# Kernel optimization log

Hardware: AMD Instinct MI355X
Metric: run time of the kernel (lower is better)

Reference implementation:

```python
import jax, jax.numpy as jnp
import numpy as np

L, B, E, H = 1024, 8, 1024, 16


def setup_inputs() -> dict:
    key = jax.random.key(0)
    k1, k2, k3, k4, k5 = jax.random.split(key, 5)
    scale = 1.0 / np.sqrt(E)
    return {
        "x": jax.random.normal(k1, (L, B, E), dtype=jnp.float32),
        "in_proj_weight": jax.random.normal(k2, (3 * E, E), dtype=jnp.float32) * scale,
        "in_proj_bias": jax.random.normal(k3, (3 * E,), dtype=jnp.float32) * 0.01,
        "out_proj_weight": jax.random.normal(k4, (E, E), dtype=jnp.float32) * scale,
        "out_proj_bias": jax.random.normal(k5, (E,), dtype=jnp.float32) * 0.01,
        "num_heads": H,
    }


def reference(x, in_proj_weight, in_proj_bias, out_proj_weight, out_proj_bias, num_heads):
    # x: [L, B, E] (tgt_len, batch, embed_dim), self-attention path of
    # multi_head_attention_func (no masks, no bias_k/v, no add_zero_attn,
    # dropout_p=0 / eval mode).
    Lq, Bq, Eq = x.shape
    hd = Eq // num_heads
    scaling = float(hd) ** -0.5
    # fused qkv projection: linear(x, in_proj_weight, in_proj_bias).chunk(3)
    qkv = x @ in_proj_weight.T + in_proj_bias  # [L, B, 3E]
    q, k, v = jnp.split(qkv, 3, axis=-1)
    q = q * scaling
    def to_heads(t):  # [L, B, E] -> [B*H, L, hd]
        return t.reshape(Lq, Bq * num_heads, hd).transpose(1, 0, 2)
    q, k, v = to_heads(q), to_heads(k), to_heads(v)
    # explicit QK^T -> softmax -> PV (naive attention, as in the source)
    scores = jnp.einsum('bqd,bkd->bqk', q, k)      # [B*H, L, L]
    attn = jax.nn.softmax(scores, axis=-1)
    out = jnp.einsum('bqk,bkd->bqd', attn, v)      # [B*H, L, hd]
    out = out.transpose(1, 0, 2).reshape(Lq, Bq, Eq)
    out = out @ out_proj_weight.T + out_proj_bias  # [L, B, E]
    return out
```

## Files before the change

### kernel.cpp

```cpp
#include <hip/hip_runtime.h>

#define L_DIM 1024
#define B_DIM 8
#define E_DIM 1024
#define H_DIM 16
#define HD 64
#define BH_DIM (B_DIM * H_DIM)

typedef float f32x4 __attribute__((ext_vector_type(4)));
typedef _Float16 f16_t;
typedef f16_t f16x4 __attribute__((ext_vector_type(4)));
typedef f16_t f16x8 __attribute__((ext_vector_type(8)));

static __device__ __forceinline__ void gld16(const void* g, void* l) {
  __builtin_amdgcn_global_load_lds(
      (const __attribute__((address_space(1))) unsigned int*)g,
      (__attribute__((address_space(3))) unsigned int*)l, 16, 0, 0);
}

__global__ __launch_bounds__(256) void convert_f16(
    const float* __restrict__ x, const float* __restrict__ wi,
    const float* __restrict__ wo, f16_t* __restrict__ x16,
    f16_t* __restrict__ wi16, f16_t* __restrict__ wo16) {
  const int NX = (L_DIM * B_DIM * E_DIM) / 4;
  const int NWI = (3 * E_DIM * E_DIM) / 4;
  const int NWO = (E_DIM * E_DIM) / 4;
  const int total = NX + NWI + NWO;
  for (int i = blockIdx.x * blockDim.x + threadIdx.x; i < total;
       i += gridDim.x * blockDim.x) {
    const float4* src; f16_t* dst; int j;
    if (i < NX)            { src = (const float4*)x;  dst = x16;  j = i; }
    else if (i < NX + NWI) { src = (const float4*)wi; dst = wi16; j = i - NX; }
    else                   { src = (const float4*)wo; dst = wo16; j = i - NX - NWI; }
    const float4 v = src[j];
    f16x4 h = {(f16_t)v.x, (f16_t)v.y, (f16_t)v.z, (f16_t)v.w};
    *(f16x4*)(dst + (size_t)j * 4) = h;
  }
}

template <int MODE>
__global__ __launch_bounds__(256, 2) void gemm_f16(
    const f16_t* __restrict__ A, const f16_t* __restrict__ B,
    const float* __restrict__ bias, void* __restrict__ O0v,
    void* __restrict__ O1v, void* __restrict__ O2v) {
  constexpr int K = 1024;
  __shared__ __align__(16) f16_t As[128 * 32];
  __shared__ __align__(16) f16_t Bs[128 * 32];

  const int tid = threadIdx.x;
  const int lane = tid & 63;
  const int wave = tid >> 6;
  const int wm = (wave & 1) * 64;
  const int wn = (wave >> 1) * 64;
  const int quad = lane >> 4;
  const int l16 = lane & 15;
  const int m0 = blockIdx.y * 128;
  const int n0 = blockIdx.x * 128;

  const int cr = tid >> 2;
  const int cc = (tid & 3) * 8;

  f32x4 acc[4][4] = {};

  for (int k0 = 0; k0 < K; k0 += 32) {
    __syncthreads();
    gld16(A + (size_t)(m0 + cr) * K + k0 + cc,      As + tid * 8);
    gld16(A + (size_t)(m0 + 64 + cr) * K + k0 + cc, As + 2048 + tid * 8);
    gld16(B + (size_t)(n0 + cr) * K + k0 + cc,      Bs + tid * 8);
    gld16(B + (size_t)(n0 + 64 + cr) * K + k0 + cc, Bs + 2048 + tid * 8);
    __syncthreads();

    f16x8 af[4], bf[4];
#pragma unroll
    for (int t = 0; t < 4; ++t) {
      af[t] = *(const f16x8*)&As[(wm + t * 16 + l16) * 32 + quad * 8];
      bf[t] = *(const f16x8*)&Bs[(wn + t * 16 + l16) * 32 + quad * 8];
    }
#pragma unroll
    for (int i = 0; i < 4; ++i)
#pragma unroll
      for (int j = 0; j < 4; ++j)
        acc[i][j] = __builtin_amdgcn_mfma_f32_16x16x32_f16(af[i], bf[j], acc[i][j], 0, 0, 0);
  }

#pragma unroll
  for (int i = 0; i < 4; ++i) {
    const int mbase = m0 + wm + i * 16 + quad * 4;
#pragma unroll
    for (int j = 0; j < 4; ++j) {
      const int n = n0 + wn + j * 16 + l16;
      const float bv = bias[n];
      if (MODE == 0) {
        f16_t* O0 = (f16_t*)O0v; f16_t* O1 = (f16_t*)O1v; f16_t* O2 = (f16_t*)O2v;
        const int chunk = n >> 10;
        const int e = n & 1023;
        const int h = e >> 6;
        const int d = e & 63;
#pragma unroll
        for (int r = 0; r < 4; ++r) {
          const int m = mbase + r;
          const int l = m >> 3, b = m & 7;
          const size_t idx = ((size_t)(b * H_DIM + h) * L_DIM + l) * HD + d;
          const float val = acc[i][j][r] + bv;
          if (chunk == 0)      O0[idx] = (f16_t)(val * 0.125f);
          else if (chunk == 1) O1[idx] = (f16_t)val;
          else                 O2[idx] = (f16_t)val;
        }
      } else {
        float* O0 = (float*)O0v;
#pragma unroll
        for (int r = 0; r < 4; ++r) {
          const int m = mbase + r;
          O0[(size_t)m * E_DIM + n] = acc[i][j][r] + bv;
        }
      }
    }
  }
}

__global__ __launch_bounds__(256, 2) void attn_f16(
    const f16_t* __restrict__ Q, const f16_t* __restrict__ K,
    const f16_t* __restrict__ V, f16_t* __restrict__ O) {
  constexpr int KSTR = 70;
  __shared__ __align__(16) f16_t Ks[64 * KSTR];
  __shared__ __align__(16) f16_t Vs[64 * KSTR];
  __shared__ float Ls[4][64];

  const int tid = threadIdx.x;
  const int lane = tid & 63;
  const int w = tid >> 6;
  const int quad = lane >> 4;
  const int l16 = lane & 15;
  const int bh = blockIdx.y;
  const int q0 = blockIdx.x * 256 + w * 64;

  const f16_t* Qb = Q + (size_t)bh * L_DIM * HD;
  const f16_t* Kb = K + (size_t)bh * L_DIM * HD;
  const f16_t* Vb = V + (size_t)bh * L_DIM * HD;

  f16x8 qf[4][2];
#pragma unroll
  for (int nt = 0; nt < 4; ++nt)
#pragma unroll
    for (int kc = 0; kc < 2; ++kc)
      qf[nt][kc] = *(const f16x8*)(Qb + (size_t)(q0 + nt * 16 + l16) * HD + kc * 32 + quad * 8);

  f32x4 oacc[4][4] = {};
  float rsum[4] = {0.0f, 0.0f, 0.0f, 0.0f};

  const int sr = tid >> 3;
  const int sc8 = (tid & 7) * 8;
  const int va = tid & 31;
  const int vg = tid >> 5;
  const int rA = (l16 >> 2) * 8 + (l16 & 3);

  for (int kt = 0; kt < 16; ++kt) {
    __syncthreads();
    {
      const f16_t* kp = Kb + (size_t)(kt * 64) * HD;
#pragma unroll
      for (int rr = 0; rr < 2; ++rr) {
        const int row = sr + rr * 32;
        *(f16x8*)&Ks[row * KSTR + sc8] = *(const f16x8*)(kp + (size_t)row * HD + sc8);
      }
      const f16_t* vp = Vb + (size_t)(kt * 64 + vg * 8) * HD + 2 * va;
      unsigned int vd[8];
#pragma unroll
      for (int i = 0; i < 8; ++i) vd[i] = *(const unsigned int*)(vp + (size_t)i * HD);
      union { unsigned int u[4]; f16x8 v; } lo, hi;
#pragma unroll
      for (int i = 0; i < 4; ++i) {
        lo.u[i] = (vd[2 * i] & 0xffffu) | (vd[2 * i + 1] << 16);
        hi.u[i] = (vd[2 * i] >> 16) | (vd[2 * i + 1] & 0xffff0000u);
      }
      *(f16x8*)&Vs[(2 * va) * KSTR + vg * 8] = lo.v;
      *(f16x8*)&Vs[(2 * va + 1) * KSTR + vg * 8] = hi.v;
    }
    __syncthreads();

#pragma unroll
    for (int c = 0; c < 2; ++c) {
      f32x4 sc[2][4] = {};
#pragma unroll
      for (int h = 0; h < 2; ++h) {
        const int row = c * 32 + h * 4 + rA;
#pragma unroll
        for (int kc = 0; kc < 2; ++kc) {
          const f16x8 ka = *(const f16x8*)&Ks[row * KSTR + kc * 32 + quad * 8];
#pragma unroll
          for (int nt = 0; nt < 4; ++nt)
            sc[h][nt] = __builtin_amdgcn_mfma_f32_16x16x32_f16(ka, qf[nt][kc], sc[h][nt], 0, 0, 0);
        }
      }

      f16x8 pa[4];
#pragma unroll
      for (int nt = 0; nt < 4; ++nt)
#pragma unroll
        for (int h = 0; h < 2; ++h)
#pragma unroll
          for (int r = 0; r < 4; ++r) {
            const float e = __expf(sc[h][nt][r]);
            rsum[nt] += e;
            pa[nt][h * 4 + r] = (f16_t)e;
          }

#pragma unroll
      for (int nd = 0; nd < 4; ++nd) {
        const f16x8 vb = *(const f16x8*)&Vs[(nd * 16 + l16) * KSTR + c * 32 + quad * 8];
#pragma unroll
        for (int nt = 0; nt < 4; ++nt)
          oacc[nt][nd] = __builtin_amdgcn_mfma_f32_16x16x32_f16(pa[nt], vb, oacc[nt][nd], 0, 0, 0);
      }
    }
  }

#pragma unroll
  for (int nt = 0; nt < 4; ++nt) {
    float rs = rsum[nt];
    rs += __shfl_xor(rs, 16); rs += __shfl_xor(rs, 32);
    if (quad == 0) Ls[w][nt * 16 + l16] = rs;
  }
  asm volatile("s_waitcnt lgkmcnt(0)" ::: "memory");

  const int b = bh >> 4;
  const int h = bh & 15;
#pragma unroll
  for (int nt = 0; nt < 4; ++nt)
#pragma unroll
    for (int r = 0; r < 4; ++r) {
      const int ql = nt * 16 + quad * 4 + r;
      const float inv = 1.0f / Ls[w][ql];
      const int qrow = q0 + ql;
#pragma unroll
      for (int nd = 0; nd < 4; ++nd) {
        const int d = nd * 16 + l16;
        O[((size_t)qrow * B_DIM + b) * E_DIM + h * HD + d] = (f16_t)(oacc[nt][nd][r] * inv);
      }
    }
}

extern "C" void kernel_launch(void* const* d_in, const int* in_sizes, int n_in,
                              void* d_out, int out_size, void* d_ws, size_t ws_size,
                              hipStream_t stream) {
  const float* x     = (const float*)d_in[0];
  const float* w_in  = (const float*)d_in[1];
  const float* b_in  = (const float*)d_in[2];
  const float* w_out = (const float*)d_in[3];
  const float* b_out = (const float*)d_in[4];

  const size_t TS = (size_t)BH_DIM * L_DIM * HD;
  f16_t* q16  = (f16_t*)d_ws;
  f16_t* k16  = q16 + TS;
  f16_t* v16  = k16 + TS;
  f16_t* x16  = v16 + TS;
  f16_t* wi16 = x16 + TS;
  f16_t* wo16 = wi16 + (size_t)3 * E_DIM * E_DIM;
  f16_t* ao16 = x16;

  convert_f16<<<4096, 256, 0, stream>>>(x, w_in, w_out, x16, wi16, wo16);
  gemm_f16<0><<<dim3(24, 64), 256, 0, stream>>>(x16, wi16, b_in, q16, k16, v16);
  attn_f16<<<dim3(4, 128), 256, 0, stream>>>(q16, k16, v16, ao16);
  gemm_f16<1><<<dim3(8, 64), 256, 0, stream>>>(ao16, wo16, b_out, d_out, nullptr, nullptr);
}
```

Measured before the change: 239.7 us.

## Add a pipelined 256x256-tile QKV GEMM with swizzled double-buffered LDS

Replaces the 128x128 QKV projection GEMM with a new 512-thread kernel. Each block computes a 256x256 tile with a K step of 64, using double-buffered LDS filled by asynchronous global_load_lds. Loads for the next tile are interleaved with MFMA phases, gated by vmcnt waits and barriers, with s_setprio raised around the MFMA bursts. It also XOR-swizzles LDS to avoid bank conflicts and remaps block ids for better L2 locality. The aim is more operand reuse per tile and overlap of memory with compute. The cost is about 128KB of LDS per block, which limits occupancy to one block per CU, plus a more fragile hand-written barrier schedule.

```diff
diff --git a/kernel.cpp b/kernel.cpp
--- a/kernel.cpp
+++ b/kernel.cpp
@@ -38,6 +38,135 @@
   }
 }
 
+
+#define GQ_FENCE asm volatile("" ::: "memory")
+#define GQ_BARRIER do { GQ_FENCE; __builtin_amdgcn_s_barrier(); GQ_FENCE; } while (0)
+#define GQ_LGKM0 do { asm volatile("s_waitcnt lgkmcnt(0)" ::: "memory"); \
+                      __builtin_amdgcn_sched_barrier(0); } while (0)
+#define GQ_VMCNT4 asm volatile("s_waitcnt vmcnt(4)" ::: "memory")
+
+#define STAGE_A(d, ht, kt) do {                                              \
+    gld16(Asrc + (size_t)(ht) * (128 * 1024) + (kt) * 64,                    \
+          &As[(d) * 16384 + (ht) * 8192 + tid * 8]);                         \
+    gld16(Asrc + (size_t)(ht) * (128 * 1024) + 64 * 1024 + (kt) * 64,        \
+          &As[(d) * 16384 + (ht) * 8192 + 4096 + tid * 8]);                  \
+  } while (0)
+#define STAGE_B(d, ht, kt) do {                                              \
+    gld16(Bsrc + (size_t)(ht) * (128 * 1024) + (kt) * 64,                    \
+          &Bs[(d) * 16384 + (ht) * 8192 + tid * 8]);                         \
+    gld16(Bsrc + (size_t)(ht) * (128 * 1024) + 64 * 1024 + (kt) * 64,        \
+          &Bs[(d) * 16384 + (ht) * 8192 + 4096 + tid * 8]);                  \
+  } while (0)
+
+static __device__ __forceinline__ const f16x8* fp16frag(
+    const f16_t* tile, int r, int ks, int quad, int l16) {
+  const int bo = (r * 128 + ks * 64 + quad * 16) ^ ((l16 & 7) << 4);
+  return (const f16x8*)((const char*)tile + bo);
+}
+
+#define GQ_PHASE(d, g, STAGE_STMT, ENDWAIT) do {                             \
+    f16x8 af_[2][2];                                                         \
+    _Pragma("unroll") for (int f_ = 0; f_ < 2; ++f_)                         \
+      _Pragma("unroll") for (int ks_ = 0; ks_ < 2; ++ks_)                    \
+        af_[f_][ks_] = *fp16frag(&As[(d) * 16384],                           \
+            wr * 128 + ((g) * 2 + f_) * 16 + l16, ks_, quad, l16);           \
+    if ((g) == 0) {                                                          \
+      _Pragma("unroll") for (int c_ = 0; c_ < 4; ++c_)                       \
+        _Pragma("unroll") for (int ks_ = 0; ks_ < 2; ++ks_)                  \
+          bf[c_][ks_] = *fp16frag(&Bs[(d) * 16384],                          \
+              wc * 64 + c_ * 16 + l16, ks_, quad, l16);                      \
+    }                                                                        \
+    STAGE_STMT;                                                              \
+    GQ_BARRIER;                                                              \
+    GQ_LGKM0;                                                                \
+    __builtin_amdgcn_s_setprio(1);                                           \
+    _Pragma("unroll") for (int f_ = 0; f_ < 2; ++f_)                         \
+      _Pragma("unroll") for (int c_ = 0; c_ < 4; ++c_)                       \
+        _Pragma("unroll") for (int ks_ = 0; ks_ < 2; ++ks_)                  \
+          acc[(g) * 2 + f_][c_] = __builtin_amdgcn_mfma_f32_16x16x32_f16(    \
+              af_[f_][ks_], bf[c_][ks_], acc[(g) * 2 + f_][c_], 0, 0, 0);    \
+    __builtin_amdgcn_s_setprio(0);                                           \
+    ENDWAIT;                                                                 \
+    GQ_BARRIER;                                                              \
+  } while (0)
+
+__global__ __launch_bounds__(512, 2) void gemm_qkv(
+    const f16_t* __restrict__ A, const f16_t* __restrict__ B,
+    const float* __restrict__ bias, f16_t* __restrict__ Oq,
+    f16_t* __restrict__ Ok, f16_t* __restrict__ Ov) {
+  constexpr int K = 1024;
+  constexpr int NT = K / 64;
+  __shared__ __align__(16) f16_t As[2 * 16384];
+  __shared__ __align__(16) f16_t Bs[2 * 16384];
+
+  const int tid = threadIdx.x;
+  const int lane = tid & 63;
+  const int w = tid >> 6;
+  const int wr = w >> 2;
+  const int wc = w & 3;
+  const int quad = lane >> 4;
+  const int l16 = lane & 15;
+
+  const int bid = blockIdx.x;
+  const int wg = (bid & 7) * 48 + (bid >> 3);
+  const int tn = wg >> 5;
+  const int tm = wg & 31;
+  const int m0 = tm * 256;
+  const int n0 = tn * 256;
+
+  const int srow = tid >> 3;
+  const int scol = ((tid & 7) ^ (srow & 7)) * 8;
+  const f16_t* Asrc = A + (size_t)(m0 + srow) * K + scol;
+  const f16_t* Bsrc = B + (size_t)(n0 + srow) * K + scol;
+
+  f32x4 acc[8][4] = {};
+  f16x8 bf[4][2];
+
+  STAGE_A(0, 0, 0); STAGE_A(0, 1, 0);
+  STAGE_B(0, 0, 0); STAGE_B(0, 1, 0);
+  STAGE_B(1, 0, 1); STAGE_B(1, 1, 1);
+  GQ_VMCNT4;
+  GQ_BARRIER;
+
+  for (int it = 0; it < 8; ++it) {
+    const int t1 = 2 * it + 1;
+    const int ta = (2 * it + 2 < NT) ? 2 * it + 2 : NT - 1;
+    const int tb = (2 * it + 3 < NT) ? 2 * it + 3 : NT - 1;
+    GQ_PHASE(0, 0, STAGE_A(1, 0, t1), );
+    GQ_PHASE(0, 1, STAGE_A(1, 1, t1), );
+    GQ_PHASE(0, 2, STAGE_B(0, 0, ta), );
+    GQ_PHASE(0, 3, STAGE_B(0, 1, ta), GQ_VMCNT4);
+    GQ_PHASE(1, 0, STAGE_A(0, 0, ta), );
+    GQ_PHASE(1, 1, STAGE_A(0, 1, ta), );
+    GQ_PHASE(1, 2, STAGE_B(1, 0, tb), );
+    GQ_PHASE(1, 3, STAGE_B(1, 1, tb), GQ_VMCNT4);
+  }
+
+#pragma unroll
+  for (int i = 0; i < 8; ++i) {
+    const int mbase = m0 + wr * 128 + i * 16 + quad * 4;
+#pragma unroll
+    for (int c = 0; c < 4; ++c) {
+      const int n = n0 + wc * 64 + c * 16 + l16;
+      const float bv = bias[n];
+      const int chunk = n >> 10;
+      const int e = n & 1023;
+      const int h = e >> 6;
+      const int d = e & 63;
+#pragma unroll
+      for (int r = 0; r < 4; ++r) {
+        const int m = mbase + r;
+        const int l = m >> 3, b = m & 7;
+        const size_t idx = ((size_t)(b * H_DIM + h) * L_DIM + l) * HD + d;
+        const float val = acc[i][c][r] + bv;
+        if (chunk == 0)      Oq[idx] = (f16_t)(val * 0.125f);
+        else if (chunk == 1) Ok[idx] = (f16_t)val;
+        else                 Ov[idx] = (f16_t)val;
+      }
+    }
+  }
+}
+
 template <int MODE>
 __global__ __launch_bounds__(256, 2) void gemm_f16(
     const f16_t* __restrict__ A, const f16_t* __restrict__ B,
@@ -70,17 +199,17 @@
     gld16(B + (size_t)(n0 + 64 + cr) * K + k0 + cc, Bs + 2048 + tid * 8);
     __syncthreads();
 
-    f16x8 af[4], bf[4];
+    f16x8 af[4], bfr[4];
 #pragma unroll
     for (int t = 0; t < 4; ++t) {
-      af[t] = *(const f16x8*)&As[(wm + t * 16 + l16) * 32 + quad * 8];
-      bf[t] = *(const f16x8*)&Bs[(wn + t * 16 + l16) * 32 + quad * 8];
+      af[t]  = *(const f16x8*)&As[(wm + t * 16 + l16) * 32 + quad * 8];
+      bfr[t] = *(const f16x8*)&Bs[(wn + t * 16 + l16) * 32 + quad * 8];
     }
 #pragma unroll
     for (int i = 0; i < 4; ++i)
 #pragma unroll
       for (int j = 0; j < 4; ++j)
-        acc[i][j] = __builtin_amdgcn_mfma_f32_16x16x32_f16(af[i], bf[j], acc[i][j], 0, 0, 0);
+        acc[i][j] = __builtin_amdgcn_mfma_f32_16x16x32_f16(af[i], bfr[j], acc[i][j], 0, 0, 0);
   }
 
 #pragma unroll
@@ -259,7 +388,7 @@
   f16_t* ao16 = x16;
 
   convert_f16<<<4096, 256, 0, stream>>>(x, w_in, w_out, x16, wi16, wo16);
-  gemm_f16<0><<<dim3(24, 64), 256, 0, stream>>>(x16, wi16, b_in, q16, k16, v16);
+  gemm_qkv<<<384, 512, 0, stream>>>(x16, wi16, b_in, q16, k16, v16);
   attn_f16<<<dim3(4, 128), 256, 0, stream>>>(q16, k16, v16, ao16);
   gemm_f16<1><<<dim3(8, 64), 256, 0, stream>>>(ao16, wo16, b_out, d_out, nullptr, nullptr);
 }
```

After: 240.7 us. No clear change (+0.4%).

## Add double-buffered swizzled QKV GEMM with XCD-aware tile mapping

Applied to the files above, without the earlier changes.

Replaces the QKV projection GEMM with a new kernel that uses BK=64 tiles, two LDS buffers with async global-to-LDS prefetch two stages ahead, XOR-swizzled LDS layout to avoid bank conflicts, MFMA priority raising, and a block-id remap that groups M tiles per XCD for L2 reuse. The aim is to hide global load latency behind MFMA work and improve cache locality in the largest GEMM. It doubles LDS use per block (64KB), which may limit occupancy to the two blocks the launch bounds request.

```diff
diff --git a/kernel.cpp b/kernel.cpp
--- a/kernel.cpp
+++ b/kernel.cpp
@@ -38,6 +38,117 @@
   }
 }
 
+
+#define GQ_FENCE asm volatile("" ::: "memory")
+#define GQ_BARRIER do { GQ_FENCE; __builtin_amdgcn_s_barrier(); GQ_FENCE; } while (0)
+#define VMW(n) asm volatile("s_waitcnt vmcnt(" #n ")" ::: "memory")
+
+static __device__ __forceinline__ const f16x8* fp16frag(
+    const f16_t* tile, int r, int ks, int quad, int l16) {
+  const int bo = (r * 128 + ks * 64 + quad * 16) ^ ((l16 & 7) << 4);
+  return (const f16x8*)((const char*)tile + bo);
+}
+
+__global__ __launch_bounds__(256, 2) void gemm_qkv(
+    const f16_t* __restrict__ A, const f16_t* __restrict__ B,
+    const float* __restrict__ bias, f16_t* __restrict__ Oq,
+    f16_t* __restrict__ Ok, f16_t* __restrict__ Ov) {
+  constexpr int K = 1024;
+  __shared__ __align__(16) f16_t As[2 * 8192];
+  __shared__ __align__(16) f16_t Bs[2 * 8192];
+
+  const int tid = threadIdx.x;
+  const int lane = tid & 63;
+  const int w = tid >> 6;
+  const int wm = (w & 1) * 64;
+  const int wn = (w >> 1) * 64;
+  const int quad = lane >> 4;
+  const int l16 = lane & 15;
+
+  const int bid = blockIdx.x;
+  const int xcd = bid & 7;
+  const int idx = bid >> 3;
+  const int tm = xcd * 8 + (idx & 7);
+  const int tn = idx >> 3;
+  const int m0 = tm * 128;
+  const int n0 = tn * 128;
+
+  const int r8 = tid >> 3;
+  const int gsw = (tid & 7) ^ (r8 & 7);
+  const f16_t* Abase = A + (size_t)(m0 + r8) * K + gsw * 8;
+  const f16_t* Bbase = B + (size_t)(n0 + r8) * K + gsw * 8;
+
+#define STAGE(kt, d) do {                                                    \
+    _Pragma("unroll") for (int s_ = 0; s_ < 4; ++s_)                         \
+      gld16(Abase + (size_t)s_ * 32 * K + (kt) * 64,                         \
+            &As[(d) * 8192 + s_ * 2048 + tid * 8]);                          \
+    _Pragma("unroll") for (int s_ = 0; s_ < 4; ++s_)                         \
+      gld16(Bbase + (size_t)s_ * 32 * K + (kt) * 64,                         \
+            &Bs[(d) * 8192 + s_ * 2048 + tid * 8]);                          \
+  } while (0)
+
+  f32x4 acc[4][4] = {};
+
+  STAGE(0, 0);
+  STAGE(1, 1);
+
+#pragma unroll
+  for (int t = 0; t < 16; ++t) {
+    const int d = t & 1;
+    VMW(8);
+    GQ_BARRIER;
+
+    f16x8 af[4][2], bf[4][2];
+#pragma unroll
+    for (int i = 0; i < 4; ++i)
+#pragma unroll
+      for (int ks = 0; ks < 2; ++ks) {
+        af[i][ks] = *fp16frag(&As[d * 8192], wm + i * 16 + l16, ks, quad, l16);
+        bf[i][ks] = *fp16frag(&Bs[d * 8192], wn + i * 16 + l16, ks, quad, l16);
+      }
+
+    __builtin_amdgcn_s_setprio(1);
+#pragma unroll
+    for (int i = 0; i < 4; ++i)
+#pragma unroll
+      for (int j = 0; j < 4; ++j)
+#pragma unroll
+        for (int ks = 0; ks < 2; ++ks)
+          acc[i][j] = __builtin_amdgcn_mfma_f32_16x16x32_f16(
+              af[i][ks], bf[j][ks], acc[i][j], 0, 0, 0);
+    __builtin_amdgcn_s_setprio(0);
+
+    GQ_BARRIER;
+    const int kt2 = (t + 2 < 16) ? t + 2 : 15;
+    STAGE(kt2, d);
+  }
+
+#pragma unroll
+  for (int i = 0; i < 4; ++i) {
+    const int mbase = m0 + wm + i * 16 + quad * 4;
+#pragma unroll
+    for (int c = 0; c < 4; ++c) {
+      const int n = n0 + wn + c * 16 + l16;
+      const float bv = bias[n];
+      const int chunk = n >> 10;
+      const int e = n & 1023;
+      const int h = e >> 6;
+      const int dd = e & 63;
+#pragma unroll
+      for (int r = 0; r < 4; ++r) {
+        const int m = mbase + r;
+        const int l = m >> 3, b = m & 7;
+        const size_t idxo = ((size_t)(b * H_DIM + h) * L_DIM + l) * HD + dd;
+        const float val = acc[i][c][r] + bv;
+        if (chunk == 0)      Oq[idxo] = (f16_t)(val * 0.125f);
+        else if (chunk == 1) Ok[idxo] = (f16_t)val;
+        else                 Ov[idxo] = (f16_t)val;
+      }
+    }
+  }
+#undef STAGE
+}
+
 template <int MODE>
 __global__ __launch_bounds__(256, 2) void gemm_f16(
     const f16_t* __restrict__ A, const f16_t* __restrict__ B,
@@ -70,17 +181,17 @@
     gld16(B + (size_t)(n0 + 64 + cr) * K + k0 + cc, Bs + 2048 + tid * 8);
     __syncthreads();
 
-    f16x8 af[4], bf[4];
+    f16x8 af[4], bfr[4];
 #pragma unroll
     for (int t = 0; t < 4; ++t) {
-      af[t] = *(const f16x8*)&As[(wm + t * 16 + l16) * 32 + quad * 8];
-      bf[t] = *(const f16x8*)&Bs[(wn + t * 16 + l16) * 32 + quad * 8];
+      af[t]  = *(const f16x8*)&As[(wm + t * 16 + l16) * 32 + quad * 8];
+      bfr[t] = *(const f16x8*)&Bs[(wn + t * 16 + l16) * 32 + quad * 8];
     }
 #pragma unroll
     for (int i = 0; i < 4; ++i)
 #pragma unroll
       for (int j = 0; j < 4; ++j)
-        acc[i][j] = __builtin_amdgcn_mfma_f32_16x16x32_f16(af[i], bf[j], acc[i][j], 0, 0, 0);
+        acc[i][j] = __builtin_amdgcn_mfma_f32_16x16x32_f16(af[i], bfr[j], acc[i][j], 0, 0, 0);
   }
 
 #pragma unroll
@@ -259,7 +370,7 @@
   f16_t* ao16 = x16;
 
   convert_f16<<<4096, 256, 0, stream>>>(x, w_in, w_out, x16, wi16, wo16);
-  gemm_f16<0><<<dim3(24, 64), 256, 0, stream>>>(x16, wi16, b_in, q16, k16, v16);
+  gemm_qkv<<<1536, 256, 0, stream>>>(x16, wi16, b_in, q16, k16, v16);
   attn_f16<<<dim3(4, 128), 256, 0, stream>>>(q16, k16, v16, ao16);
   gemm_f16<1><<<dim3(8, 64), 256, 0, stream>>>(ao16, wo16, b_out, d_out, nullptr, nullptr);
 }
```

Result: faster. 226.6 us (-5.4%).
